# Kernel optimization log

Hardware: AMD Instinct MI355X
Metric: run time of the kernel (lower is better)

## Reference

```python
import jax, jax.numpy as jnp
from jax import lax
import numpy as np

ALIVE_THRESHOLD = 0.1


def make_percept_kernel(C):
    # 5 fixed 3x3x3 depthwise filters per channel: identity, neighbor-sum, sobel x/y/z
    ident = np.zeros((3, 3, 3), np.float32); ident[1, 1, 1] = 1.0
    nsum = np.ones((3, 3, 3), np.float32); nsum[1, 1, 1] = 0.0; nsum /= 26.0
    smooth = np.array([1.0, 2.0, 1.0], np.float32) / 4.0
    deriv = np.array([-1.0, 0.0, 1.0], np.float32) / 2.0
    gx = np.einsum('i,j,k->ijk', deriv, smooth, smooth)
    gy = np.einsum('i,j,k->ijk', smooth, deriv, smooth)
    gz = np.einsum('i,j,k->ijk', smooth, smooth, deriv)
    filt = np.stack([ident, nsum, gx, gy, gz])            # (5,3,3,3)
    k = np.tile(filt[None], (C, 1, 1, 1, 1))              # (C,5,3,3,3) group-major
    return jnp.asarray(k.reshape(C * 5, 1, 3, 3, 3))      # OIDHW, groups=C


def setup_inputs() -> dict:
    key = jax.random.key(0)
    ks = jax.random.split(key, 6)
    B, C, D = 2, 16, 64
    hidden, n_filt = 128, 5
    state = jax.random.uniform(ks[0], (B, C, D, D, D), dtype=jnp.float32) * 0.5
    w_percept = make_percept_kernel(C)                    # (5C,1,3,3,3) fixed
    w1 = jax.random.normal(ks[1], (hidden, n_filt * C), dtype=jnp.float32) * 0.05
    b1 = jnp.zeros((hidden,), jnp.float32)
    w2 = jax.random.normal(ks[2], (C, hidden), dtype=jnp.float32) * 0.05
    b2 = jnp.zeros((C,), jnp.float32)
    return {"state": state, "w_percept": w_percept, "w1": w1, "b1": b1,
            "w2": w2, "b2": b2, "steps": 2}


def _alive_mask(s):
    # alpha is the last channel; 3x3x3 local max > threshold
    alpha = s[:, -1:]
    m = lax.reduce_window(alpha, -jnp.inf, lax.max,
                          (1, 1, 3, 3, 3), (1, 1, 1, 1, 1), 'SAME')
    return m > ALIVE_THRESHOLD


def reference(state, w_percept, w1, b1, w2, b2, steps):
    C = state.shape[1]

    def step(s):
        pre_life = _alive_mask(s)
        perceived = lax.conv_general_dilated(
            s, w_percept, (1, 1, 1), 'SAME',
            dimension_numbers=('NCDHW', 'OIDHW', 'NCDHW'),
            feature_group_count=C)                        # (B,5C,D,H,W)
        h = jax.nn.relu(jnp.einsum('bcdhw,oc->bodhw', perceived, w1)
                        + b1[None, :, None, None, None])
        dx = (jnp.einsum('bcdhw,oc->bodhw', h, w2)
              + b2[None, :, None, None, None])
        new_s = s + dx
        post_life = _alive_mask(new_s)
        life = (pre_life & post_life).astype(s.dtype)
        return jnp.clip(new_s * life, -1.0, 1.0)

    for _ in range(steps):
        state = step(state)
    return state
```

## Files before the change

### kernel.cpp

```cpp
#include <hip/hip_runtime.h>

typedef _Float16 f16;
typedef _Float16 h2    __attribute__((ext_vector_type(2)));
typedef _Float16 f16x8 __attribute__((ext_vector_type(8)));
typedef float    f32x4 __attribute__((ext_vector_type(4)));
typedef unsigned int uint;

#define D3   (64*64*64)
#define CC   16
#define NVOX (2*D3)

#define OFF_TA  (NVOX * 32)
#define OFF_M   (OFF_TA + NVOX * 4)
#define OFF_W1H (OFF_M + NVOX)
#define OFF_W2H (OFF_W1H + 128 * 96 * 2)

#define ROWB 208

static __device__ __forceinline__ uint pkbits(float lo, float hi) {
    return __builtin_bit_cast(uint, __builtin_amdgcn_cvt_pkrtz(lo, hi));
}
static __device__ __forceinline__ uint pkrne(float lo, float hi) {
    return __builtin_bit_cast(uint, h2{(f16)lo, (f16)hi});
}
static __device__ __forceinline__ f16x8 bc8(uint4 u) {
    return __builtin_bit_cast(f16x8, u);
}
static __device__ __forceinline__ h2 bch(uint u) {
    return __builtin_bit_cast(h2, u);
}
static __device__ __forceinline__ uint hbits(h2 v) {
    return __builtin_bit_cast(uint, v);
}
static __device__ __forceinline__ f32x4 mfma16(f16x8 a, f16x8 b, f32x4 c) {
    return __builtin_amdgcn_mfma_f32_16x16x32_f16(a, b, c, 0, 0, 0);
}
static __device__ __forceinline__ float clip1(float v) {
    return fminf(fmaxf(v, -1.f), 1.f);
}

__global__ __launch_bounds__(256) void prep_kernel(
    const float* __restrict__ st,
    const float* __restrict__ w1,
    const float* __restrict__ b1,
    const float* __restrict__ w2,
    uint4* __restrict__ S, float* __restrict__ SA,
    f16* __restrict__ w1h, f16* __restrict__ w2h)
{
    const int id = blockIdx.x * blockDim.x + threadIdx.x;
    const int b = id >> 18, vox = id & (D3 - 1);
    const float* __restrict__ p = st + (size_t)b * CC * D3 + vox;
    float v[16];
    #pragma unroll
    for (int c = 0; c < 16; ++c) v[c] = p[c * D3];
    S[id * 2 + 0] = make_uint4(pkrne(v[0], v[1]),  pkrne(v[2], v[3]),
                               pkrne(v[4], v[5]),  pkrne(v[6], v[7]));
    S[id * 2 + 1] = make_uint4(pkrne(v[8], v[9]),  pkrne(v[10], v[11]),
                               pkrne(v[12], v[13]), pkrne(v[14], v[15]));
    SA[id] = v[15];

    if (blockIdx.x == 0) {
        const int t = threadIdx.x;
        for (int i = t; i < 128 * 96; i += 256) {
            const int j = i / 96, k = i - j * 96;
            float w;
            if (k < 80) {
                const int c2 = k / 10, rem = k - c2 * 10, q = rem >> 1, par = rem & 1;
                w = w1[j * 80 + (2 * c2 + par) * 5 + q];
            } else if (k == 80) w = b1[j];
            else w = 0.f;
            w1h[i] = (f16)w;
        }
        for (int i = t; i < 16 * 128; i += 256) w2h[i] = (f16)w2[i];
    }
}

__global__ __launch_bounds__(256, 3) void nca_update_kernel(
    const uint4* __restrict__ Sv,
    const float* __restrict__ SA,
    const f16*  __restrict__ w1h,
    const f16*  __restrict__ w2h,
    const float* __restrict__ b2,
    uint2* __restrict__ Tw,
    float* __restrict__ TA,
    unsigned char* __restrict__ pre_mask)
{
    __shared__ __align__(16) char arena[256 * ROWB];

    const int hw = blockIdx.x;
    const int logical = (hw & 7) * 256 + (hw >> 3);
    const int bx = logical & 7, by = (logical >> 3) & 7;
    const int bz = (logical >> 6) & 15, b = logical >> 10;
    const int t  = threadIdx.x;

    uint4* stH0 = (uint4*)arena;
    uint4* stH1 = stH0 + 600;
    float* stAl = (float*)(arena + 2 * 600 * 16);

    {
        const int gx0 = bx * 8 - 1, gy0 = by * 8 - 1, gz0 = bz * 4 - 1;
        for (int r = t; r < 600; r += 256) {
            const int lx = r % 10, ly = (r / 10) % 10, lz = r / 100;
            const int gx = gx0 + lx, gy = gy0 + ly, gz = gz0 + lz;
            const bool ok = ((unsigned)gx < 64u) & ((unsigned)gy < 64u) & ((unsigned)gz < 64u);
            const int gv = (b << 18) + (gz << 12) + (gy << 6) + gx;
            const uint4 z4 = make_uint4(0u, 0u, 0u, 0u);
            stH0[r] = ok ? Sv[gv * 2 + 0] : z4;
            stH1[r] = ok ? Sv[gv * 2 + 1] : z4;
            stAl[r] = ok ? SA[gv] : 0.f;
        }
    }
    __syncthreads();

    const int lx = t & 7, ly = (t >> 3) & 7, lz = t >> 6;

    h2 sumv[8], gxv[8], gyv[8], gzv[8], ctrv[8];
    #pragma unroll
    for (int k = 0; k < 8; ++k) {
        sumv[k] = h2{(f16)0.f, (f16)0.f};
        gxv[k] = sumv[k]; gyv[k] = sumv[k]; gzv[k] = sumv[k];
    }

    #pragma unroll
    for (int dz = -1; dz <= 1; ++dz) {
        const float wz_s = (dz == 0) ? 0.5f : 0.25f;
        const float wz_d = (dz == 0) ? 0.f  : (dz < 0 ? -0.5f : 0.5f);
        #pragma unroll
        for (int dy = -1; dy <= 1; ++dy) {
            const float wy_s = (dy == 0) ? 0.5f : 0.25f;
            const float wy_d = (dy == 0) ? 0.f  : (dy < 0 ? -0.5f : 0.5f);
            const int rowu = (lz + 1 + dz) * 100 + (ly + 1 + dy) * 10;
            #pragma unroll
            for (int dxx = -1; dxx <= 1; ++dxx) {
                const float wx_s = (dxx == 0) ? 0.5f : 0.25f;
                const float wx_d = (dxx == 0) ? 0.f  : (dxx < 0 ? -0.5f : 0.5f);
                const float wgx = wz_d * wy_s * wx_s;
                const float wgy = wz_s * wy_d * wx_s;
                const float wgz = wz_s * wy_s * wx_d;
                const int u = rowu + lx + 1 + dxx;
                const uint4 q0 = stH0[u];
                const uint4 q1 = stH1[u];
                const uint uu[8] = {q0.x, q0.y, q0.z, q0.w, q1.x, q1.y, q1.z, q1.w};
                #pragma unroll
                for (int k = 0; k < 8; ++k) {
                    const h2 v = bch(uu[k]);
                    sumv[k] += v;
                    if (wgx != 0.f) gxv[k] += h2{(f16)wgx, (f16)wgx} * v;
                    if (wgy != 0.f) gyv[k] += h2{(f16)wgy, (f16)wgy} * v;
                    if (wgz != 0.f) gzv[k] += h2{(f16)wgz, (f16)wgz} * v;
                    if (dz == 0 && dy == 0 && dxx == 0) ctrv[k] = v;
                }
            }
        }
    }

    {
        float amax = -1e30f;
        #pragma unroll
        for (int dz = -1; dz <= 1; ++dz)
            #pragma unroll
            for (int dy = -1; dy <= 1; ++dy)
                #pragma unroll
                for (int dxx = -1; dxx <= 1; ++dxx)
                    amax = fmaxf(amax, stAl[(lz + 1 + dz) * 100 + (ly + 1 + dy) * 10 +
                                            (lx + 1 + dxx)]);
        const int gvox = ((bz * 4 + lz) << 12) + ((by * 8 + ly) << 6) + (bx * 8 + lx);
        pre_mask[(b << 18) + gvox] = (amax > 0.1f) ? (unsigned char)1 : (unsigned char)0;
    }

    uint pp[40];
    {
        const h2 inv26 = h2{(f16)(1.f / 26.f), (f16)(1.f / 26.f)};
        #pragma unroll
        for (int k = 0; k < 8; ++k) {
            pp[k * 5 + 0] = hbits(ctrv[k]);
            pp[k * 5 + 1] = hbits((sumv[k] - ctrv[k]) * inv26);
            pp[k * 5 + 2] = hbits(gxv[k]);
            pp[k * 5 + 3] = hbits(gyv[k]);
            pp[k * 5 + 4] = hbits(gzv[k]);
        }
    }

    __syncthreads();

    {
        char* prow = arena + t * ROWB;
        #pragma unroll
        for (int c = 0; c < 10; ++c) {
            *(uint4*)(prow + 16 * c) =
                make_uint4(pp[4 * c], pp[4 * c + 1], pp[4 * c + 2], pp[4 * c + 3]);
        }
        *(uint4*)(prow + 160) = make_uint4(0x3C00u, 0u, 0u, 0u);
        *(uint4*)(prow + 176) = make_uint4(0u, 0u, 0u, 0u);
    }
    asm volatile("" ::: "memory");

    const int lane = t & 63, wave = t >> 6;
    const int n = lane & 15, g = lane >> 4;

    uint4 sfr[3];
    {
        const int ko = 10 * (n >> 1) + (n & 1);
        #pragma unroll
        for (int ks = 0; ks < 3; ++ks) {
            const int j = ko - 32 * ks - 8 * g;
            uint4 u = make_uint4(0u, 0u, 0u, 0u);
            if (j >= 0 && j < 8) {
                const uint val = 0x3C00u << ((j & 1) * 16);
                const int w = j >> 1;
                if      (w == 0) u.x = val;
                else if (w == 1) u.y = val;
                else if (w == 2) u.z = val;
                else             u.w = val;
            }
            sfr[ks] = u;
        }
    }
    const float b2v0 = b2[4 * g + 0], b2v1 = b2[4 * g + 1];
    const float b2v2 = b2[4 * g + 2], b2v3 = b2[4 * g + 3];

    #pragma unroll
    for (int bi = 0; bi < 2; ++bi) {
        char* rp0 = arena + ((4 * wave + 2 * bi + 0) * 16 + n) * ROWB;
        char* rp1 = arena + ((4 * wave + 2 * bi + 1) * 16 + n) * ROWB;

        const f16x8 B00 = bc8(*(const uint4*)(rp0       + 16 * g));
        const f16x8 B01 = bc8(*(const uint4*)(rp0 + 64  + 16 * g));
        const f16x8 B02 = bc8(*(const uint4*)(rp0 + 128 + 16 * g));
        const f16x8 B10 = bc8(*(const uint4*)(rp1       + 16 * g));
        const f16x8 B11 = bc8(*(const uint4*)(rp1 + 64  + 16 * g));
        const f16x8 B12 = bc8(*(const uint4*)(rp1 + 128 + 16 * g));

        f32x4 acc0 = {0.f, 0.f, 0.f, 0.f}, acc1v = {0.f, 0.f, 0.f, 0.f};
        acc0  = mfma16(bc8(sfr[0]), B00, acc0);
        acc0  = mfma16(bc8(sfr[1]), B01, acc0);
        acc0  = mfma16(bc8(sfr[2]), B02, acc0);
        acc1v = mfma16(bc8(sfr[0]), B10, acc1v);
        acc1v = mfma16(bc8(sfr[1]), B11, acc1v);
        acc1v = mfma16(bc8(sfr[2]), B12, acc1v);

        #pragma unroll
        for (int half = 0; half < 2; ++half) {
            f32x4 h0[4], h1[4];
            #pragma unroll
            for (int ht = 0; ht < 4; ++ht) {
                h0[ht] = (f32x4){0.f, 0.f, 0.f, 0.f};
                h1[ht] = (f32x4){0.f, 0.f, 0.f, 0.f};
            }
            #pragma unroll
            for (int ks = 0; ks < 3; ++ks) {
                const f16x8 Bk0 = (ks == 0) ? B00 : (ks == 1) ? B01 : B02;
                const f16x8 Bk1 = (ks == 0) ? B10 : (ks == 1) ? B11 : B12;
                #pragma unroll
                for (int ht = 0; ht < 4; ++ht) {
                    const f16x8 A = *(const f16x8*)(w1h +
                        (size_t)(64 * half + 16 * ht + n) * 96 + 32 * ks + 8 * g);
                    h0[ht] = mfma16(A, Bk0, h0[ht]);
                    h1[ht] = mfma16(A, Bk1, h1[ht]);
                }
            }
            #pragma unroll
            for (int ht = 0; ht < 4; ++ht) {
                *(uint2*)(rp0 + 32 * ht + 8 * g) = make_uint2(
                    pkbits(fmaxf(h0[ht][0], 0.f), fmaxf(h0[ht][1], 0.f)),
                    pkbits(fmaxf(h0[ht][2], 0.f), fmaxf(h0[ht][3], 0.f)));
                *(uint2*)(rp1 + 32 * ht + 8 * g) = make_uint2(
                    pkbits(fmaxf(h1[ht][0], 0.f), fmaxf(h1[ht][1], 0.f)),
                    pkbits(fmaxf(h1[ht][2], 0.f), fmaxf(h1[ht][3], 0.f)));
            }
            asm volatile("" ::: "memory");
            #pragma unroll
            for (int k2 = 0; k2 < 2; ++k2) {
                const f16x8 A2 = *(const f16x8*)(w2h + n * 128 + 64 * half + 32 * k2 + 8 * g);
                acc0  = mfma16(A2, bc8(*(const uint4*)(rp0 + 64 * k2 + 16 * g)), acc0);
                acc1v = mfma16(A2, bc8(*(const uint4*)(rp1 + 64 * k2 + 16 * g)), acc1v);
            }
            asm volatile("" ::: "memory");
        }

        #pragma unroll
        for (int ii = 0; ii < 2; ++ii) {
            const f32x4 a = (ii == 0) ? acc0 : acc1v;
            const int lv = (4 * wave + 2 * bi + ii) * 16 + n;
            const int gvox = ((bz * 4 + (lv >> 6)) << 12) +
                             ((by * 8 + ((lv >> 3) & 7)) << 6) + (bx * 8 + (lv & 7));
            const int gv = (b << 18) + gvox;
            const float c0 = a[0] + b2v0, c1 = a[1] + b2v1;
            const float c2 = a[2] + b2v2, c3 = a[3] + b2v3;
            Tw[gv * 4 + g] = make_uint2(pkrne(c0, c1), pkrne(c2, c3));
            if (g == 3) TA[gv] = c3;
        }
    }
}

__global__ __launch_bounds__(256) void mask_clip_kernel(
    const uint4* __restrict__ T,
    const float* __restrict__ TA,
    const unsigned char* __restrict__ pre_mask,
    uint4* __restrict__ S,
    float* __restrict__ SA,
    float* __restrict__ out,
    const int final_pass)
{
    const int id = blockIdx.x * blockDim.x + threadIdx.x;
    const int x = id & 63;
    const int y = (id >> 6) & 63;
    const int z = (id >> 12) & 63;
    const int b = id >> 18;
    const float* __restrict__ ta = TA + (b << 18);

    float amax = -1e30f;
    #pragma unroll
    for (int dz = -1; dz <= 1; ++dz) {
        #pragma unroll
        for (int dy = -1; dy <= 1; ++dy) {
            #pragma unroll
            for (int dxx = -1; dxx <= 1; ++dxx) {
                const int zz = z + dz, yy = y + dy, xx = x + dxx;
                const bool ok = ((unsigned)zz < 64u) & ((unsigned)yy < 64u) &
                                ((unsigned)xx < 64u);
                if (ok) amax = fmaxf(amax, ta[(zz << 12) + (yy << 6) + xx]);
            }
        }
    }

    const float lf = (amax > 0.1f && pre_mask[id]) ? 1.f : 0.f;

    const uint4 q0 = T[id * 2 + 0];
    const uint4 q1 = T[id * 2 + 1];
    const uint w[8] = {q0.x, q0.y, q0.z, q0.w, q1.x, q1.y, q1.z, q1.w};
    float v[16];
    #pragma unroll
    for (int wi = 0; wi < 8; ++wi) {
        const h2 hv = bch(w[wi]);
        v[2 * wi + 0] = clip1((float)hv[0] * lf);
        v[2 * wi + 1] = clip1((float)hv[1] * lf);
    }

    if (!final_pass) {
        S[id * 2 + 0] = make_uint4(pkrne(v[0], v[1]),  pkrne(v[2], v[3]),
                                   pkrne(v[4], v[5]),  pkrne(v[6], v[7]));
        S[id * 2 + 1] = make_uint4(pkrne(v[8], v[9]),  pkrne(v[10], v[11]),
                                   pkrne(v[12], v[13]), pkrne(v[14], v[15]));
        SA[id] = clip1(ta[id & (D3 - 1)] * lf);
    } else {
        const int vox = id & (D3 - 1);
        float* __restrict__ ob = out + (size_t)b * CC * D3 + vox;
        #pragma unroll
        for (int c = 0; c < 16; ++c) ob[c * D3] = v[c];
    }
}

extern "C" void kernel_launch(void* const* d_in, const int* in_sizes, int n_in,
                              void* d_out, int out_size, void* d_ws, size_t ws_size,
                              hipStream_t stream)
{
    const float* state = (const float*)d_in[0];
    const float* w1 = (const float*)d_in[2];
    const float* b1 = (const float*)d_in[3];
    const float* w2 = (const float*)d_in[4];
    const float* b2 = (const float*)d_in[5];

    char* ws = (char*)d_ws;
    uint2*         T   = (uint2*)ws;
    float*         TA  = (float*)(ws + OFF_TA);
    unsigned char* M   = (unsigned char*)(ws + OFF_M);
    f16*           W1H = (f16*)(ws + OFF_W1H);
    f16*           W2H = (f16*)(ws + OFF_W2H);

    float* out = (float*)d_out;
    uint4* S   = (uint4*)d_out;
    float* SA  = (float*)((char*)d_out + NVOX * 32);

    prep_kernel<<<NVOX / 256, 256, 0, stream>>>(state, w1, b1, w2, S, SA, W1H, W2H);

    dim3 ugrid(2048), ublock(256);
    dim3 mgrid(NVOX / 256), mblock(256);

    nca_update_kernel<<<ugrid, ublock, 0, stream>>>(S, SA, W1H, W2H, b2, T, TA, M);
    mask_clip_kernel<<<mgrid, mblock, 0, stream>>>((const uint4*)T, TA, M, S, SA, out, 0);
    nca_update_kernel<<<ugrid, ublock, 0, stream>>>(S, SA, W1H, W2H, b2, T, TA, M);
    mask_clip_kernel<<<mgrid, mblock, 0, stream>>>((const uint4*)T, TA, M, S, SA, out, 1);
}
```

Before: 162.1 us.

## Fuse step-1 mask/clip into step-2 update halo load, tile final mask kernel

Removes the intermediate mask_clip pass after the first update. The second update kernel now loads the raw update output, the alpha field with a 2-voxel halo and the pre-mask, and applies the alive mask and clip in shared memory before computing perception. Buffers ping-pong between the workspace and the output buffer. The final mask kernel is tiled so its alpha max uses a shared-memory halo. This saves one full-volume read and write round trip at the cost of redundant halo masking work and more shared memory per block.

```diff
diff --git a/kernel.cpp b/kernel.cpp
--- a/kernel.cpp
+++ b/kernel.cpp
@@ -5,15 +5,16 @@
 typedef _Float16 f16x8 __attribute__((ext_vector_type(8)));
 typedef float    f32x4 __attribute__((ext_vector_type(4)));
 typedef unsigned int uint;
+typedef unsigned char uchar;
 
 #define D3   (64*64*64)
 #define CC   16
 #define NVOX (2*D3)
 
-#define OFF_TA  (NVOX * 32)
-#define OFF_M   (OFF_TA + NVOX * 4)
-#define OFF_W1H (OFF_M + NVOX)
-#define OFF_W2H (OFF_W1H + 128 * 96 * 2)
+#define WS_TA   (NVOX * 32)
+#define WS_M    (WS_TA + NVOX * 4)
+#define WS_W1H  (WS_M + NVOX)
+#define WS_W2H  (WS_W1H + 128 * 96 * 2)
 
 #define ROWB 208
 
@@ -75,15 +76,17 @@
     }
 }
 
-__global__ __launch_bounds__(256, 3) void nca_update_kernel(
-    const uint4* __restrict__ Sv,
-    const float* __restrict__ SA,
+__global__ __launch_bounds__(256, 3) void nca_fused_kernel(
+    const uint4* __restrict__ Tin,
+    const float* __restrict__ Ain,
+    const uchar* __restrict__ Min,
     const f16*  __restrict__ w1h,
     const f16*  __restrict__ w2h,
     const float* __restrict__ b2,
-    uint2* __restrict__ Tw,
-    float* __restrict__ TA,
-    unsigned char* __restrict__ pre_mask)
+    uint2* __restrict__ Tout,
+    float* __restrict__ Aout,
+    uchar* __restrict__ Mout,
+    const int apply_mask)
 {
     __shared__ __align__(16) char arena[256 * ROWB];
 
@@ -95,22 +98,68 @@
 
     uint4* stH0 = (uint4*)arena;
     uint4* stH1 = stH0 + 600;
-    float* stAl = (float*)(arena + 2 * 600 * 16);
-
-    {
-        const int gx0 = bx * 8 - 1, gy0 = by * 8 - 1, gz0 = bz * 4 - 1;
+    float* stAl = (float*)(arena + 19200);
+    float* TAh  = (float*)(arena + 21600);
+    uchar* Mh   = (uchar*)(arena + 26208);
+
+    const int gx0 = bx * 8 - 1, gy0 = by * 8 - 1, gz0 = bz * 4 - 1;
+
+    for (int r = t; r < 600; r += 256) {
+        const int lx = r % 10, ly = (r / 10) % 10, lz = r / 100;
+        const int gx = gx0 + lx, gy = gy0 + ly, gz = gz0 + lz;
+        const bool ok = ((unsigned)gx < 64u) & ((unsigned)gy < 64u) & ((unsigned)gz < 64u);
+        const int gv = (b << 18) + (gz << 12) + (gy << 6) + gx;
+        const uint4 z4 = make_uint4(0u, 0u, 0u, 0u);
+        stH0[r] = ok ? Tin[gv * 2 + 0] : z4;
+        stH1[r] = ok ? Tin[gv * 2 + 1] : z4;
+        if (!apply_mask) stAl[r] = ok ? Ain[gv] : 0.f;
+        else             Mh[r]   = ok ? Min[gv] : (uchar)0;
+    }
+    if (apply_mask) {
+        for (int r = t; r < 1152; r += 256) {
+            const int i = r % 12, j = (r / 12) % 12, k = r / 144;
+            const int gx = gx0 - 1 + i, gy = gy0 - 1 + j, gz = gz0 - 1 + k;
+            const bool ok = ((unsigned)gx < 64u) & ((unsigned)gy < 64u) & ((unsigned)gz < 64u);
+            TAh[r] = ok ? Ain[(b << 18) + (gz << 12) + (gy << 6) + gx] : 0.f;
+        }
+    }
+    __syncthreads();
+
+    if (apply_mask) {
         for (int r = t; r < 600; r += 256) {
             const int lx = r % 10, ly = (r / 10) % 10, lz = r / 100;
             const int gx = gx0 + lx, gy = gy0 + ly, gz = gz0 + lz;
             const bool ok = ((unsigned)gx < 64u) & ((unsigned)gy < 64u) & ((unsigned)gz < 64u);
-            const int gv = (b << 18) + (gz << 12) + (gy << 6) + gx;
-            const uint4 z4 = make_uint4(0u, 0u, 0u, 0u);
-            stH0[r] = ok ? Sv[gv * 2 + 0] : z4;
-            stH1[r] = ok ? Sv[gv * 2 + 1] : z4;
-            stAl[r] = ok ? SA[gv] : 0.f;
-        }
-    }
-    __syncthreads();
+            float al = 0.f;
+            if (ok) {
+                const int ti = (lz + 1) * 144 + (ly + 1) * 12 + (lx + 1);
+                float amax = -1e30f;
+                #pragma unroll
+                for (int dz = -1; dz <= 1; ++dz)
+                    #pragma unroll
+                    for (int dy = -1; dy <= 1; ++dy)
+                        #pragma unroll
+                        for (int dxx = -1; dxx <= 1; ++dxx)
+                            amax = fmaxf(amax, TAh[ti + dz * 144 + dy * 12 + dxx]);
+                const float lf = (amax > 0.1f && Mh[r]) ? 1.f : 0.f;
+                const uint4 q0 = stH0[r];
+                const uint4 q1 = stH1[r];
+                const uint w8[8] = {q0.x, q0.y, q0.z, q0.w, q1.x, q1.y, q1.z, q1.w};
+                uint o8[8];
+                #pragma unroll
+                for (int wi = 0; wi < 8; ++wi) {
+                    const h2 hv = bch(w8[wi]);
+                    o8[wi] = pkrne(clip1((float)hv[0] * lf),
+                                   clip1((float)hv[1] * lf));
+                }
+                stH0[r] = make_uint4(o8[0], o8[1], o8[2], o8[3]);
+                stH1[r] = make_uint4(o8[4], o8[5], o8[6], o8[7]);
+                al = clip1(TAh[ti] * lf);
+            }
+            stAl[r] = al;
+        }
+        __syncthreads();
+    }
 
     const int lx = t & 7, ly = (t >> 3) & 7, lz = t >> 6;
 
@@ -165,7 +214,7 @@
                     amax = fmaxf(amax, stAl[(lz + 1 + dz) * 100 + (ly + 1 + dy) * 10 +
                                             (lx + 1 + dxx)]);
         const int gvox = ((bz * 4 + lz) << 12) + ((by * 8 + ly) << 6) + (bx * 8 + lx);
-        pre_mask[(b << 18) + gvox] = (amax > 0.1f) ? (unsigned char)1 : (unsigned char)0;
+        Mout[(b << 18) + gvox] = (amax > 0.1f) ? (uchar)1 : (uchar)0;
     }
 
     uint pp[40];
@@ -287,67 +336,57 @@
             const int gv = (b << 18) + gvox;
             const float c0 = a[0] + b2v0, c1 = a[1] + b2v1;
             const float c2 = a[2] + b2v2, c3 = a[3] + b2v3;
-            Tw[gv * 4 + g] = make_uint2(pkrne(c0, c1), pkrne(c2, c3));
-            if (g == 3) TA[gv] = c3;
-        }
-    }
-}
-
-__global__ __launch_bounds__(256) void mask_clip_kernel(
+            Tout[gv * 4 + g] = make_uint2(pkrne(c0, c1), pkrne(c2, c3));
+            if (g == 3) Aout[gv] = c3;
+        }
+    }
+}
+
+__global__ __launch_bounds__(256) void mc_final_kernel(
     const uint4* __restrict__ T,
     const float* __restrict__ TA,
-    const unsigned char* __restrict__ pre_mask,
-    uint4* __restrict__ S,
-    float* __restrict__ SA,
-    float* __restrict__ out,
-    const int final_pass)
+    const uchar* __restrict__ M,
+    float* __restrict__ out)
 {
-    const int id = blockIdx.x * blockDim.x + threadIdx.x;
-    const int x = id & 63;
-    const int y = (id >> 6) & 63;
-    const int z = (id >> 12) & 63;
-    const int b = id >> 18;
-    const float* __restrict__ ta = TA + (b << 18);
-
+    __shared__ float sAl[600];
+
+    const int bid = blockIdx.x;
+    const int bx = bid & 7, by = (bid >> 3) & 7;
+    const int bz = (bid >> 6) & 15, b = bid >> 10;
+    const int t  = threadIdx.x;
+
+    const int gx0 = bx * 8 - 1, gy0 = by * 8 - 1, gz0 = bz * 4 - 1;
+    for (int r = t; r < 600; r += 256) {
+        const int lx = r % 10, ly = (r / 10) % 10, lz = r / 100;
+        const int gx = gx0 + lx, gy = gy0 + ly, gz = gz0 + lz;
+        const bool ok = ((unsigned)gx < 64u) & ((unsigned)gy < 64u) & ((unsigned)gz < 64u);
+        sAl[r] = ok ? TA[(b << 18) + (gz << 12) + (gy << 6) + gx] : 0.f;
+    }
+    __syncthreads();
+
+    const int lx = t & 7, ly = (t >> 3) & 7, lz = t >> 6;
     float amax = -1e30f;
     #pragma unroll
-    for (int dz = -1; dz <= 1; ++dz) {
-        #pragma unroll
-        for (int dy = -1; dy <= 1; ++dy) {
-            #pragma unroll
-            for (int dxx = -1; dxx <= 1; ++dxx) {
-                const int zz = z + dz, yy = y + dy, xx = x + dxx;
-                const bool ok = ((unsigned)zz < 64u) & ((unsigned)yy < 64u) &
-                                ((unsigned)xx < 64u);
-                if (ok) amax = fmaxf(amax, ta[(zz << 12) + (yy << 6) + xx]);
-            }
-        }
-    }
-
-    const float lf = (amax > 0.1f && pre_mask[id]) ? 1.f : 0.f;
-
-    const uint4 q0 = T[id * 2 + 0];
-    const uint4 q1 = T[id * 2 + 1];
-    const uint w[8] = {q0.x, q0.y, q0.z, q0.w, q1.x, q1.y, q1.z, q1.w};
-    float v[16];
-    #pragma unroll
-    for (int wi = 0; wi < 8; ++wi) {
-        const h2 hv = bch(w[wi]);
-        v[2 * wi + 0] = clip1((float)hv[0] * lf);
-        v[2 * wi + 1] = clip1((float)hv[1] * lf);
-    }
-
-    if (!final_pass) {
-        S[id * 2 + 0] = make_uint4(pkrne(v[0], v[1]),  pkrne(v[2], v[3]),
-                                   pkrne(v[4], v[5]),  pkrne(v[6], v[7]));
-        S[id * 2 + 1] = make_uint4(pkrne(v[8], v[9]),  pkrne(v[10], v[11]),
-                                   pkrne(v[12], v[13]), pkrne(v[14], v[15]));
-        SA[id] = clip1(ta[id & (D3 - 1)] * lf);
-    } else {
-        const int vox = id & (D3 - 1);
-        float* __restrict__ ob = out + (size_t)b * CC * D3 + vox;
-        #pragma unroll
-        for (int c = 0; c < 16; ++c) ob[c * D3] = v[c];
+    for (int dz = -1; dz <= 1; ++dz)
+        #pragma unroll
+        for (int dy = -1; dy <= 1; ++dy)
+            #pragma unroll
+            for (int dxx = -1; dxx <= 1; ++dxx)
+                amax = fmaxf(amax, sAl[(lz + 1 + dz) * 100 + (ly + 1 + dy) * 10 +
+                                        (lx + 1 + dxx)]);
+
+    const int gvox = ((bz * 4 + lz) << 12) + ((by * 8 + ly) << 6) + (bx * 8 + lx);
+    const int gv = (b << 18) + gvox;
+    const float lf = (amax > 0.1f && M[gv]) ? 1.f : 0.f;
+
+    const uint4 q0 = T[gv * 2 + 0];
+    const uint4 q1 = T[gv * 2 + 1];
+    const uint w8[8] = {q0.x, q0.y, q0.z, q0.w, q1.x, q1.y, q1.z, q1.w};
+    float* __restrict__ ob = out + (size_t)b * CC * D3 + gvox;
+    #pragma unroll
+    for (int c = 0; c < 16; ++c) {
+        const h2 hv = bch(w8[c >> 1]);
+        ob[c * D3] = clip1((float)hv[c & 1] * lf);
     }
 }
 
@@ -361,24 +400,28 @@
     const float* w2 = (const float*)d_in[4];
     const float* b2 = (const float*)d_in[5];
 
-    char* ws = (char*)d_ws;
-    uint2*         T   = (uint2*)ws;
-    float*         TA  = (float*)(ws + OFF_TA);
-    unsigned char* M   = (unsigned char*)(ws + OFF_M);
-    f16*           W1H = (f16*)(ws + OFF_W1H);
-    f16*           W2H = (f16*)(ws + OFF_W2H);
-
-    float* out = (float*)d_out;
-    uint4* S   = (uint4*)d_out;
-    float* SA  = (float*)((char*)d_out + NVOX * 32);
+    char* ws  = (char*)d_ws;
+    char* doc = (char*)d_out;
+
+    uint4* S   = (uint4*)ws;
+    float* SA  = (float*)(ws + WS_TA);
+    uint2* T2w = (uint2*)ws;
+    float* TA2 = (float*)(ws + WS_TA);
+    uchar* M2  = (uchar*)(ws + WS_M);
+    f16*   W1H = (f16*)(ws + WS_W1H);
+    f16*   W2H = (f16*)(ws + WS_W2H);
+
+    uint2* T1w = (uint2*)doc;
+    float* TA1 = (float*)(doc + NVOX * 32);
+    uchar* M1  = (uchar*)(doc + NVOX * 36);
+    float* out = (float*)doc;
 
     prep_kernel<<<NVOX / 256, 256, 0, stream>>>(state, w1, b1, w2, S, SA, W1H, W2H);
 
-    dim3 ugrid(2048), ublock(256);
-    dim3 mgrid(NVOX / 256), mblock(256);
-
-    nca_update_kernel<<<ugrid, ublock, 0, stream>>>(S, SA, W1H, W2H, b2, T, TA, M);
-    mask_clip_kernel<<<mgrid, mblock, 0, stream>>>((const uint4*)T, TA, M, S, SA, out, 0);
-    nca_update_kernel<<<ugrid, ublock, 0, stream>>>(S, SA, W1H, W2H, b2, T, TA, M);
-    mask_clip_kernel<<<mgrid, mblock, 0, stream>>>((const uint4*)T, TA, M, S, SA, out, 1);
-}
+    dim3 grid(2048), block(256);
+    nca_fused_kernel<<<grid, block, 0, stream>>>(S, SA, (const uchar*)nullptr,
+                                                 W1H, W2H, b2, T1w, TA1, M1, 0);
+    nca_fused_kernel<<<grid, block, 0, stream>>>((const uint4*)T1w, TA1, M1,
+                                                 W1H, W2H, b2, T2w, TA2, M2, 1);
+    mc_final_kernel<<<grid, block, 0, stream>>>((const uint4*)T2w, TA2, M2, out);
+}
```

Result: no change. 159.3 us (-1.7%).
